# Performance work log

Hardware: AMD Instinct MI355X
Metric: run time of the kernel (lower is better)

## Reference

```python
import jax, jax.numpy as jnp
import numpy as np

MAGNITUDE = 9
PROB = 0.5
WARP_STRENGTH = MAGNITUDE * 0.3 / 9.0  # = 0.3


def _notaknot_matrix(S):
    # System for second derivatives M of a cubic spline on uniform grid h=1
    # (scipy CubicSpline default bc_type='not-a-knot').
    A = np.zeros((S, S), dtype=np.float32)
    i = np.arange(1, S - 1)
    A[i, i - 1] = 1.0
    A[i, i] = 4.0
    A[i, i + 1] = 1.0
    # not-a-knot: third derivative continuous at x1 and x_{S-2}
    A[0, 0], A[0, 1], A[0, 2] = 1.0, -2.0, 1.0
    A[-1, -3], A[-1, -2], A[-1, -1] = 1.0, -2.0, 1.0
    return A


def setup_inputs() -> dict:
    key = jax.random.key(0)
    k1, k2, k3 = jax.random.split(key, 3)
    B, C, S = 128, 64, 4096
    x = jax.random.normal(k1, (B, C, S), dtype=jnp.float32)
    # per-sample scale ~ U(1 - warp_strength, 1 + warp_strength)
    scale = (1.0 - WARP_STRENGTH) + 2.0 * WARP_STRENGTH * jax.random.uniform(k2, (B,), dtype=jnp.float32)
    # per-sample apply decision: rand < prob
    apply_mask = jax.random.uniform(k3, (B,)) < PROB
    return {"x": x, "scale": scale, "apply_mask": apply_mask}


def reference(x, scale, apply_mask):
    B, C, S = x.shape
    A = jnp.asarray(_notaknot_matrix(S))  # (S, S), fixed uniform-grid system

    # --- fit not-a-knot cubic splines for all B*C signals at once ---
    y = x.reshape(B * C, S)
    rhs = jnp.zeros_like(y).at[:, 1:-1].set(
        6.0 * (y[:, :-2] - 2.0 * y[:, 1:-1] + y[:, 2:])
    )  # not-a-knot rows have rhs 0
    M = jnp.linalg.solve(A, rhs.T).T.reshape(B, C, S)  # second derivatives

    # --- warped evaluation points (shared across channels of a sample) ---
    grid = jnp.arange(S, dtype=x.dtype)
    w = jnp.clip(grid[None, :] * scale[:, None], 0.0, S - 1)  # (B, S)
    idx = jnp.clip(jnp.floor(w).astype(jnp.int32), 0, S - 2)  # interval index
    t = (w - idx.astype(x.dtype))[:, None, :]                 # (B, 1, S)

    idx3 = jnp.broadcast_to(idx[:, None, :], (B, C, S))
    y0 = jnp.take_along_axis(x, idx3, axis=2)
    y1 = jnp.take_along_axis(x, idx3 + 1, axis=2)
    M0 = jnp.take_along_axis(M, idx3, axis=2)
    M1 = jnp.take_along_axis(M, idx3 + 1, axis=2)

    # s(t) = y0 + b t + c t^2 + d t^3 on each unit interval (h = 1)
    b = (y1 - y0) - (2.0 * M0 + M1) / 6.0
    c = M0 / 2.0
    d = (M1 - M0) / 6.0
    warped = y0 + t * (b + t * (c + t * d))

    return jnp.where(apply_mask[:, None, None], warped, x)
```

## Files before the change

### kernel.cpp

```cpp
#include <hip/hip_runtime.h>
#include <math.h>


#define SLEN 4096
#define WRAD 8
#define WC   6
#define BLK  1024

typedef float f32x4 __attribute__((ext_vector_type(4)));

__global__ __launch_bounds__(BLK, 8) void time_warp_kernel(
    const float* __restrict__ x,
    const float* __restrict__ scale,
    const int*   __restrict__ apply_mask,
    float* __restrict__ out,
    int C)
{
    __shared__ float  sy[SLEN];
    __shared__ float2 sym2[SLEN];

    const int bid = blockIdx.x;
    const int b   = bid / C;
    const int t   = threadIdx.x;
    const float* __restrict__ xin = x   + (size_t)bid * SLEN;
    float*       __restrict__ o   = out + (size_t)bid * SLEN;

    if (apply_mask[b] == 0) {
        const f32x4* __restrict__ xi4 = (const f32x4*)xin;
        f32x4*       __restrict__ o4  = (f32x4*)o;
        f32x4 v = xi4[t];
        __builtin_nontemporal_store(v, &o4[t]);
        return;
    }

    {
        const float4* __restrict__ xi4 = (const float4*)xin;
        *(float4*)&sy[4 * t] = xi4[t];
    }
    __syncthreads();

    const float r = 0.26794919243112270f;
    float G[WRAD + 1];
    G[0] = 0.28867513459481287f;
    #pragma unroll
    for (int k = 1; k <= WRAD; ++k) G[k] = -G[k - 1] * r;
    float Hh[WC + 2];
    Hh[0] = 12.0f * (G[1] - G[0]);
    #pragma unroll
    for (int k = 1; k < WC; ++k) Hh[k] = 6.0f * (G[k - 1] - 2.0f * G[k] + G[k + 1]);
    Hh[WC]     = 6.0f * (G[WC - 1] - 2.0f * G[WC]);
    Hh[WC + 1] = 6.0f * G[WC];
    const float log2r = -1.8999686269529532f;

    {
        const int j0 = 4 * t;
        if (j0 >= 36 && j0 <= SLEN - 44) {
            float wv[20];
            #pragma unroll
            for (int m = 0; m < 5; ++m)
                *(float4*)&wv[4 * m] = *(const float4*)&sy[j0 - 8 + 4 * m];
            float mv[4];
            #pragma unroll
            for (int e = 0; e < 4; ++e) {
                float acc = Hh[0] * wv[8 + e];
                #pragma unroll
                for (int k = 1; k <= WC + 1; ++k)
                    acc += Hh[k] * (wv[8 + e - k] + wv[8 + e + k]);
                mv[e] = acc;
            }
            *(float4*)&sym2[j0]     = make_float4(wv[8],  mv[0], wv[9],  mv[1]);
            *(float4*)&sym2[j0 + 2] = make_float4(wv[10], mv[2], wv[11], mv[3]);
        } else {
            const float M1  = sy[0]        - 2.0f * sy[1]        + sy[2];
            const float MS2 = sy[SLEN - 3] - 2.0f * sy[SLEN - 2] + sy[SLEN - 1];

            float v1 = 0.0f, vS2 = 0.0f;
            #pragma unroll
            for (int k = 1; k <= WRAD; ++k) {
                const int ja = 1 + k;
                float fa = 6.0f * (sy[ja - 1] - 2.0f * sy[ja] + sy[ja + 1]);
                if (ja == 2) fa -= M1;
                v1 += G[k] * fa;
                const int jb = SLEN - 2 - k;
                float fb = 6.0f * (sy[jb - 1] - 2.0f * sy[jb] + sy[jb + 1]);
                if (jb == SLEN - 3) fb -= MS2;
                vS2 += G[k] * fb;
            }

            float wv[28];
            #pragma unroll
            for (int m = 0; m < 7; ++m) {
                const int q = j0 - 12 + 4 * m;
                float4 v = make_float4(0.0f, 0.0f, 0.0f, 0.0f);
                if (q >= 0 && q <= SLEN - 4) v = *(const float4*)&sy[q];
                *(float4*)&wv[4 * m] = v;
            }
            float fw[20];
            #pragma unroll
            for (int p = 0; p < 20; ++p) {
                const int jj = j0 + p - 8;
                float fv = 6.0f * (wv[p + 3] - 2.0f * wv[p + 4] + wv[p + 5]);
                if (jj < 2 || jj > SLEN - 3) fv = 0.0f;
                if (jj == 2)        fv -= M1;
                if (jj == SLEN - 3) fv -= MS2;
                fw[p] = fv;
            }
            float mv[4];
            #pragma unroll
            for (int e = 0; e < 4; ++e) {
                float acc = G[0] * fw[8 + e];
                #pragma unroll
                for (int k = 1; k <= WRAD; ++k)
                    acc += G[k] * (fw[8 + e - k] + fw[8 + e + k]);
                const int i = j0 + e;
                if (i >= 2 && i <= 34) {
                    float cc = v1 * exp2f((float)(i - 1) * log2r);
                    acc += (i & 1) ? -cc : cc;
                }
                if (i >= SLEN - 36 && i <= SLEN - 3) {
                    float cc = vS2 * exp2f((float)(SLEN - 2 - i) * log2r);
                    acc += (i & 1) ? cc : -cc;
                }
                mv[e] = acc;
            }
            if (j0 == 0)        { mv[1] = M1;  mv[0] = 2.0f * M1  - mv[2]; }
            if (j0 == SLEN - 4) { mv[2] = MS2; mv[3] = 2.0f * MS2 - mv[1]; }
            *(float4*)&sym2[j0]     = make_float4(wv[12], mv[0], wv[13], mv[1]);
            *(float4*)&sym2[j0 + 2] = make_float4(wv[14], mv[2], wv[15], mv[3]);
        }
    }
    __syncthreads();

    const float sc = scale[b];
    #pragma unroll
    for (int q = 0; q < 4; ++q) {
        const int j = t + BLK * q;
        float w = fminf((float)j * sc, (float)(SLEN - 1));
        int idx = (int)w;
        if (idx > SLEN - 2) idx = SLEN - 2;
        const float tt = w - (float)idx;
        const float2 p0 = sym2[idx];
        const float2 p1 = sym2[idx + 1];
        const float y0 = p0.x, m0 = p0.y;
        const float y1 = p1.x, m1 = p1.y;
        const float bb = (y1 - y0) - (2.0f * m0 + m1) * (1.0f / 6.0f);
        const float cc = 0.5f * m0;
        const float dd = (m1 - m0) * (1.0f / 6.0f);
        const float res = y0 + tt * (bb + tt * (cc + tt * dd));
        __builtin_nontemporal_store(res, &o[j]);
    }
}

extern "C" void kernel_launch(void* const* d_in, const int* in_sizes, int n_in,
                              void* d_out, int out_size, void* d_ws, size_t ws_size,
                              hipStream_t stream) {
    const float* x     = (const float*)d_in[0];
    const float* scale = (const float*)d_in[1];
    const int*   mask  = (const int*)d_in[2];
    float*       out   = (float*)d_out;

    const int B     = in_sizes[1];
    const int total = in_sizes[0];
    const int C     = total / (B * SLEN);
    const int nblk  = B * C;

    time_warp_kernel<<<nblk, BLK, 0, stream>>>(x, scale, mask, out, C);
}
```

Baseline: 233.8 us.

## Process two signals per block and prefetch the second during the first

Each block now handles two consecutive signals of the same sample. The second signal's global load is issued before the first signal's convolution and evaluation, so its memory latency overlaps that compute. Shared memory is split into separate y and M arrays instead of an interleaved float2 layout. The change halves the block count, which reduces launch and scheduling overhead, but it adds serialisation within each block and an extra shared buffer. It also assumes C is even so that a pair never straddles two samples.

```diff
diff --git a/kernel.cpp b/kernel.cpp
--- a/kernel.cpp
+++ b/kernel.cpp
@@ -9,36 +9,9 @@
 
 typedef float f32x4 __attribute__((ext_vector_type(4)));
 
-__global__ __launch_bounds__(BLK, 8) void time_warp_kernel(
-    const float* __restrict__ x,
-    const float* __restrict__ scale,
-    const int*   __restrict__ apply_mask,
-    float* __restrict__ out,
-    int C)
+__device__ __forceinline__ void spline_conv(const float* __restrict__ sy,
+                                            float* __restrict__ sm, int t)
 {
-    __shared__ float  sy[SLEN];
-    __shared__ float2 sym2[SLEN];
-
-    const int bid = blockIdx.x;
-    const int b   = bid / C;
-    const int t   = threadIdx.x;
-    const float* __restrict__ xin = x   + (size_t)bid * SLEN;
-    float*       __restrict__ o   = out + (size_t)bid * SLEN;
-
-    if (apply_mask[b] == 0) {
-        const f32x4* __restrict__ xi4 = (const f32x4*)xin;
-        f32x4*       __restrict__ o4  = (f32x4*)o;
-        f32x4 v = xi4[t];
-        __builtin_nontemporal_store(v, &o4[t]);
-        return;
-    }
-
-    {
-        const float4* __restrict__ xi4 = (const float4*)xin;
-        *(float4*)&sy[4 * t] = xi4[t];
-    }
-    __syncthreads();
-
     const float r = 0.26794919243112270f;
     float G[WRAD + 1];
     G[0] = 0.28867513459481287f;
@@ -52,86 +25,86 @@
     Hh[WC + 1] = 6.0f * G[WC];
     const float log2r = -1.8999686269529532f;
 
-    {
-        const int j0 = 4 * t;
-        if (j0 >= 36 && j0 <= SLEN - 44) {
-            float wv[20];
+    const int j0 = 4 * t;
+    if (j0 >= 36 && j0 <= SLEN - 44) {
+        float wv[20];
+        #pragma unroll
+        for (int m = 0; m < 5; ++m)
+            *(float4*)&wv[4 * m] = *(const float4*)&sy[j0 - 8 + 4 * m];
+        float mv[4];
+        #pragma unroll
+        for (int e = 0; e < 4; ++e) {
+            float acc = Hh[0] * wv[8 + e];
             #pragma unroll
-            for (int m = 0; m < 5; ++m)
-                *(float4*)&wv[4 * m] = *(const float4*)&sy[j0 - 8 + 4 * m];
-            float mv[4];
+            for (int k = 1; k <= WC + 1; ++k)
+                acc += Hh[k] * (wv[8 + e - k] + wv[8 + e + k]);
+            mv[e] = acc;
+        }
+        *(float4*)&sm[j0] = make_float4(mv[0], mv[1], mv[2], mv[3]);
+    } else {
+        const float M1  = sy[0]        - 2.0f * sy[1]        + sy[2];
+        const float MS2 = sy[SLEN - 3] - 2.0f * sy[SLEN - 2] + sy[SLEN - 1];
+
+        float v1 = 0.0f, vS2 = 0.0f;
+        #pragma unroll
+        for (int k = 1; k <= WRAD; ++k) {
+            const int ja = 1 + k;
+            float fa = 6.0f * (sy[ja - 1] - 2.0f * sy[ja] + sy[ja + 1]);
+            if (ja == 2) fa -= M1;
+            v1 += G[k] * fa;
+            const int jb = SLEN - 2 - k;
+            float fb = 6.0f * (sy[jb - 1] - 2.0f * sy[jb] + sy[jb + 1]);
+            if (jb == SLEN - 3) fb -= MS2;
+            vS2 += G[k] * fb;
+        }
+
+        float wv[28];
+        #pragma unroll
+        for (int m = 0; m < 7; ++m) {
+            const int q = j0 - 12 + 4 * m;
+            float4 v = make_float4(0.0f, 0.0f, 0.0f, 0.0f);
+            if (q >= 0 && q <= SLEN - 4) v = *(const float4*)&sy[q];
+            *(float4*)&wv[4 * m] = v;
+        }
+        float fw[20];
+        #pragma unroll
+        for (int p = 0; p < 20; ++p) {
+            const int jj = j0 + p - 8;
+            float fv = 6.0f * (wv[p + 3] - 2.0f * wv[p + 4] + wv[p + 5]);
+            if (jj < 2 || jj > SLEN - 3) fv = 0.0f;
+            if (jj == 2)        fv -= M1;
+            if (jj == SLEN - 3) fv -= MS2;
+            fw[p] = fv;
+        }
+        float mv[4];
+        #pragma unroll
+        for (int e = 0; e < 4; ++e) {
+            float acc = G[0] * fw[8 + e];
             #pragma unroll
-            for (int e = 0; e < 4; ++e) {
-                float acc = Hh[0] * wv[8 + e];
-                #pragma unroll
-                for (int k = 1; k <= WC + 1; ++k)
-                    acc += Hh[k] * (wv[8 + e - k] + wv[8 + e + k]);
-                mv[e] = acc;
+            for (int k = 1; k <= WRAD; ++k)
+                acc += G[k] * (fw[8 + e - k] + fw[8 + e + k]);
+            const int i = j0 + e;
+            if (i >= 2 && i <= 34) {
+                float cc = v1 * exp2f((float)(i - 1) * log2r);
+                acc += (i & 1) ? -cc : cc;
             }
-            *(float4*)&sym2[j0]     = make_float4(wv[8],  mv[0], wv[9],  mv[1]);
-            *(float4*)&sym2[j0 + 2] = make_float4(wv[10], mv[2], wv[11], mv[3]);
-        } else {
-            const float M1  = sy[0]        - 2.0f * sy[1]        + sy[2];
-            const float MS2 = sy[SLEN - 3] - 2.0f * sy[SLEN - 2] + sy[SLEN - 1];
+            if (i >= SLEN - 36 && i <= SLEN - 3) {
+                float cc = vS2 * exp2f((float)(SLEN - 2 - i) * log2r);
+                acc += (i & 1) ? cc : -cc;
+            }
+            mv[e] = acc;
+        }
+        if (j0 == 0)        { mv[1] = M1;  mv[0] = 2.0f * M1  - mv[2]; }
+        if (j0 == SLEN - 4) { mv[2] = MS2; mv[3] = 2.0f * MS2 - mv[1]; }
+        *(float4*)&sm[j0] = make_float4(mv[0], mv[1], mv[2], mv[3]);
+    }
+}
 
-            float v1 = 0.0f, vS2 = 0.0f;
-            #pragma unroll
-            for (int k = 1; k <= WRAD; ++k) {
-                const int ja = 1 + k;
-                float fa = 6.0f * (sy[ja - 1] - 2.0f * sy[ja] + sy[ja + 1]);
-                if (ja == 2) fa -= M1;
-                v1 += G[k] * fa;
-                const int jb = SLEN - 2 - k;
-                float fb = 6.0f * (sy[jb - 1] - 2.0f * sy[jb] + sy[jb + 1]);
-                if (jb == SLEN - 3) fb -= MS2;
-                vS2 += G[k] * fb;
-            }
-
-            float wv[28];
-            #pragma unroll
-            for (int m = 0; m < 7; ++m) {
-                const int q = j0 - 12 + 4 * m;
-                float4 v = make_float4(0.0f, 0.0f, 0.0f, 0.0f);
-                if (q >= 0 && q <= SLEN - 4) v = *(const float4*)&sy[q];
-                *(float4*)&wv[4 * m] = v;
-            }
-            float fw[20];
-            #pragma unroll
-            for (int p = 0; p < 20; ++p) {
-                const int jj = j0 + p - 8;
-                float fv = 6.0f * (wv[p + 3] - 2.0f * wv[p + 4] + wv[p + 5]);
-                if (jj < 2 || jj > SLEN - 3) fv = 0.0f;
-                if (jj == 2)        fv -= M1;
-                if (jj == SLEN - 3) fv -= MS2;
-                fw[p] = fv;
-            }
-            float mv[4];
-            #pragma unroll
-            for (int e = 0; e < 4; ++e) {
-                float acc = G[0] * fw[8 + e];
-                #pragma unroll
-                for (int k = 1; k <= WRAD; ++k)
-                    acc += G[k] * (fw[8 + e - k] + fw[8 + e + k]);
-                const int i = j0 + e;
-                if (i >= 2 && i <= 34) {
-                    float cc = v1 * exp2f((float)(i - 1) * log2r);
-                    acc += (i & 1) ? -cc : cc;
-                }
-                if (i >= SLEN - 36 && i <= SLEN - 3) {
-                    float cc = vS2 * exp2f((float)(SLEN - 2 - i) * log2r);
-                    acc += (i & 1) ? cc : -cc;
-                }
-                mv[e] = acc;
-            }
-            if (j0 == 0)        { mv[1] = M1;  mv[0] = 2.0f * M1  - mv[2]; }
-            if (j0 == SLEN - 4) { mv[2] = MS2; mv[3] = 2.0f * MS2 - mv[1]; }
-            *(float4*)&sym2[j0]     = make_float4(wv[12], mv[0], wv[13], mv[1]);
-            *(float4*)&sym2[j0 + 2] = make_float4(wv[14], mv[2], wv[15], mv[3]);
-        }
-    }
-    __syncthreads();
-
-    const float sc = scale[b];
+__device__ __forceinline__ void spline_eval(const float* __restrict__ sy,
+                                            const float* __restrict__ sm,
+                                            float* __restrict__ o,
+                                            float sc, int t)
+{
     #pragma unroll
     for (int q = 0; q < 4; ++q) {
         const int j = t + BLK * q;
@@ -139,16 +112,64 @@
         int idx = (int)w;
         if (idx > SLEN - 2) idx = SLEN - 2;
         const float tt = w - (float)idx;
-        const float2 p0 = sym2[idx];
-        const float2 p1 = sym2[idx + 1];
-        const float y0 = p0.x, m0 = p0.y;
-        const float y1 = p1.x, m1 = p1.y;
+        const float y0 = sy[idx];
+        const float y1 = sy[idx + 1];
+        const float m0 = sm[idx];
+        const float m1 = sm[idx + 1];
         const float bb = (y1 - y0) - (2.0f * m0 + m1) * (1.0f / 6.0f);
         const float cc = 0.5f * m0;
         const float dd = (m1 - m0) * (1.0f / 6.0f);
         const float res = y0 + tt * (bb + tt * (cc + tt * dd));
         __builtin_nontemporal_store(res, &o[j]);
     }
+}
+
+__global__ __launch_bounds__(BLK, 8) void time_warp_kernel(
+    const float* __restrict__ x,
+    const float* __restrict__ scale,
+    const int*   __restrict__ apply_mask,
+    float* __restrict__ out,
+    int C)
+{
+    __shared__ float syA[SLEN];
+    __shared__ float syB[SLEN];
+    __shared__ float sm [SLEN];
+
+    const int pid = blockIdx.x;
+    const int s0  = 2 * pid;
+    const int b   = s0 / C;
+    const int t   = threadIdx.x;
+    const float* __restrict__ xA = x   + (size_t)s0 * SLEN;
+    const float* __restrict__ xB = xA + SLEN;
+    float*       __restrict__ oA = out + (size_t)s0 * SLEN;
+    float*       __restrict__ oB = oA + SLEN;
+
+    if (apply_mask[b] == 0) {
+        f32x4 vA = ((const f32x4*)xA)[t];
+        f32x4 vB = ((const f32x4*)xB)[t];
+        __builtin_nontemporal_store(vA, &((f32x4*)oA)[t]);
+        __builtin_nontemporal_store(vB, &((f32x4*)oB)[t]);
+        return;
+    }
+
+    const float sc = scale[b];
+
+    *(float4*)&syA[4 * t] = ((const float4*)xA)[t];
+    __syncthreads();
+
+    const float4 b4 = ((const float4*)xB)[t];
+
+    spline_conv(syA, sm, t);
+    __syncthreads();
+
+    spline_eval(syA, sm, oA, sc, t);
+    *(float4*)&syB[4 * t] = b4;
+    __syncthreads();
+
+    spline_conv(syB, sm, t);
+    __syncthreads();
+
+    spline_eval(syB, sm, oB, sc, t);
 }
 
 extern "C" void kernel_launch(void* const* d_in, const int* in_sizes, int n_in,
@@ -162,7 +183,8 @@
     const int B     = in_sizes[1];
     const int total = in_sizes[0];
     const int C     = total / (B * SLEN);
-    const int nblk  = B * C;
+    const int nsig  = B * C;
+    const int nblk  = nsig / 2;
 
     time_warp_kernel<<<nblk, BLK, 0, stream>>>(x, scale, mask, out, C);
 }
```

Measured after the change: 254.7 us. +8.9%, slower.
